# Kernel optimization log

Measured on AMD Instinct MI355X. Metric: run time of the kernel, lower is better.

## Reference

```python
import jax, jax.numpy as jnp
import numpy as np

TEMPERATURE = 0.5
NEG_INF = -1e9  # used to mask self-similarity diagonal before logsumexp


def setup_inputs() -> dict:
    key = jax.random.key(0)
    k1, k2 = jax.random.split(key)
    N, Z = 4096, 128
    z1 = jax.random.normal(k1, (N, Z), dtype=jnp.float32)
    z2 = jax.random.normal(k2, (N, Z), dtype=jnp.float32)
    return {"z1": z1, "z2": z2}


def reference(z1, z2):
    # NT-Xent (SimCLR) loss. Faithful to:
    #   sim = cosine_similarity over all pairs of concat([z1, z2])
    #   positives = sim diagonals at offsets +-N; negatives = all off-(self)diag entries
    #   cross_entropy with the positive as class 0  ->  -pos/T + logsumexp(all non-self sims / T)
    N = z1.shape[0]
    reps = jnp.concatenate([z1, z2], axis=0)                      # [2N, Z]
    # row-normalize once; cosine sim matrix is then a single GEMM
    norms = jnp.linalg.norm(reps, axis=-1, keepdims=True)
    # torch cosine_similarity clamps norms by eps=1e-8
    nreps = reps / jnp.maximum(norms, 1e-8)
    sim = nreps @ nreps.T                                          # [2N, 2N]
    # positives: sim[i, i+N] for i<N and sim[i, i-N] for i>=N
    l_pos = jnp.diagonal(sim, offset=N)                            # [N]
    r_pos = jnp.diagonal(sim, offset=-N)                           # [N]
    positives = jnp.concatenate([l_pos, r_pos])                    # [2N]
    # logsumexp over all entries except the self-similarity diagonal.
    # (The positive entry stays in the denominator exactly once, matching
    #  concat([positive, negatives]) in the original.)
    two_n = 2 * N
    self_mask = jnp.eye(two_n, dtype=bool)
    logits = jnp.where(self_mask, NEG_INF, sim / TEMPERATURE)      # [2N, 2N]
    lse = jax.nn.logsumexp(logits, axis=1)                         # [2N]
    per_row = lse - positives / TEMPERATURE                        # CE with label 0
    return jnp.sum(per_row) / two_n
```

## Files before the change

kernel.cpp:

```cpp
#include <hip/hip_runtime.h>
#include <hip/hip_bf16.h>


#define N_PAIRS 4096
#define ZDIM    128
#define NROWS   8192
#define EXP_SCALE 2.8853900817779268f

typedef __bf16 bf16x8 __attribute__((ext_vector_type(8)));
typedef float  floatx4 __attribute__((ext_vector_type(4)));

__global__ __launch_bounds__(256) void k_zero(float* __restrict__ denom) {
    int i = blockIdx.x * 256 + threadIdx.x;
    if (i < NROWS) denom[i] = 0.0f;
}

__global__ __launch_bounds__(256) void k_normalize(
    const float* __restrict__ z1, const float* __restrict__ z2,
    __hip_bfloat16* __restrict__ nreps, float* __restrict__ pos)
{
    const int w = threadIdx.x >> 6;
    const int lane = threadIdx.x & 63;
    const int p = blockIdx.x * 4 + w;
    const float2 a = ((const float2*)(z1 + (size_t)p * ZDIM))[lane];
    const float2 b = ((const float2*)(z2 + (size_t)p * ZDIM))[lane];
    float s1 = a.x * a.x + a.y * a.y;
    float s2 = b.x * b.x + b.y * b.y;
    float d  = a.x * b.x + a.y * b.y;
    #pragma unroll
    for (int off = 1; off < 64; off <<= 1) {
        s1 += __shfl_xor(s1, off, 64);
        s2 += __shfl_xor(s2, off, 64);
        d  += __shfl_xor(d,  off, 64);
    }
    const float n1 = fmaxf(sqrtf(s1), 1e-8f);
    const float n2 = fmaxf(sqrtf(s2), 1e-8f);
    const float i1 = 1.0f / n1, i2 = 1.0f / n2;
    float2 na; na.x = a.x * i1; na.y = a.y * i1;
    float2 nb; nb.x = b.x * i2; nb.y = b.y * i2;
    ((__hip_bfloat162*)(nreps + (size_t)p * ZDIM))[lane] = __float22bfloat162_rn(na);
    ((__hip_bfloat162*)(nreps + (size_t)(p + N_PAIRS) * ZDIM))[lane] = __float22bfloat162_rn(nb);
    if (lane == 0) pos[p] = d * i1 * i2;
}

__global__ __launch_bounds__(256, 2) void k_simsum(
    const __hip_bfloat16* __restrict__ nreps, float* __restrict__ denom)
{
    const int tid  = threadIdx.x;
    const int lane = tid & 63;
    const int w    = tid >> 6;
    const int wr   = w >> 1, wc = w & 1;
    const int rt   = blockIdx.x >> 3;
    const int cs   = blockIdx.x & 7;
    const int q    = lane >> 4;
    const int l16  = lane & 15;

    const int arow = rt * 128 + wr * 64 + l16;
    const __hip_bfloat16* Abase = nreps + (size_t)arow * ZDIM + q * 8;
    bf16x8 afrag[4][4];
    #pragma unroll
    for (int mt = 0; mt < 4; ++mt)
        #pragma unroll
        for (int ks = 0; ks < 4; ++ks)
            afrag[mt][ks] = *(const bf16x8*)(Abase + mt * 16 * ZDIM + ks * 32);

    float rowsum[4][4];
    #pragma unroll
    for (int mt = 0; mt < 4; ++mt)
        #pragma unroll
        for (int r = 0; r < 4; ++r) rowsum[mt][r] = 0.0f;

    const int colbase = cs * 1024 + wc * 64 + l16;
    const int growb   = rt * 128 + wr * 64 + q * 4;

    for (int it = 0; it < 8; ++it) {
        floatx4 acc[4][4];
        #pragma unroll
        for (int mt = 0; mt < 4; ++mt)
            #pragma unroll
            for (int nt = 0; nt < 4; ++nt) {
                acc[mt][nt].x = 0.f; acc[mt][nt].y = 0.f;
                acc[mt][nt].z = 0.f; acc[mt][nt].w = 0.f;
            }
        const __hip_bfloat16* Bbase =
            nreps + (size_t)(colbase + it * 128) * ZDIM + q * 8;
        #pragma unroll
        for (int ks = 0; ks < 4; ++ks) {
            bf16x8 bfrag[4];
            #pragma unroll
            for (int nt = 0; nt < 4; ++nt)
                bfrag[nt] = *(const bf16x8*)(Bbase + nt * 16 * ZDIM + ks * 32);
            #pragma unroll
            for (int mt = 0; mt < 4; ++mt)
                #pragma unroll
                for (int nt = 0; nt < 4; ++nt)
                    acc[mt][nt] = __builtin_amdgcn_mfma_f32_16x16x32_bf16(
                        afrag[mt][ks], bfrag[nt], acc[mt][nt], 0, 0, 0);
        }
        const int gcolb = cs * 1024 + it * 128 + wc * 64 + l16;
        #pragma unroll
        for (int mt = 0; mt < 4; ++mt) {
            #pragma unroll
            for (int nt = 0; nt < 4; ++nt) {
                const int gcol = gcolb + nt * 16;
                #pragma unroll
                for (int r = 0; r < 4; ++r) {
                    const int grow = growb + mt * 16 + r;
                    const float e = __expf(acc[mt][nt][r] * 2.0f);
                    rowsum[mt][r] += (grow == gcol) ? 0.0f : e;
                }
            }
        }
    }

    #pragma unroll
    for (int mt = 0; mt < 4; ++mt)
        #pragma unroll
        for (int r = 0; r < 4; ++r) {
            float s = rowsum[mt][r];
            s += __shfl_xor(s, 1, 64);
            s += __shfl_xor(s, 2, 64);
            s += __shfl_xor(s, 4, 64);
            s += __shfl_xor(s, 8, 64);
            rowsum[mt][r] = s;
        }
    if (l16 == 0) {
        #pragma unroll
        for (int mt = 0; mt < 4; ++mt)
            #pragma unroll
            for (int r = 0; r < 4; ++r) {
                const int grow = rt * 128 + wr * 64 + mt * 16 + q * 4 + r;
                atomicAdd(&denom[grow], rowsum[mt][r]);
            }
    }
}

__global__ __launch_bounds__(1024) void k_finish(
    const float* __restrict__ denom, const float* __restrict__ pos,
    float* __restrict__ out)
{
    __shared__ float red[1024];
    const int t = threadIdx.x;
    float s = 0.0f;
    for (int i = t; i < NROWS; i += 1024) s += __logf(denom[i]);
    float p = 0.0f;
    for (int i = t; i < N_PAIRS; i += 1024) p += pos[i];
    red[t] = s - 4.0f * p;
    __syncthreads();
    for (int off = 512; off > 0; off >>= 1) {
        if (t < off) red[t] += red[t + off];
        __syncthreads();
    }
    if (t == 0) out[0] = red[0] / (float)NROWS;
}

extern "C" void kernel_launch(void* const* d_in, const int* in_sizes, int n_in,
                              void* d_out, int out_size, void* d_ws, size_t ws_size,
                              hipStream_t stream) {
    const float* z1 = (const float*)d_in[0];
    const float* z2 = (const float*)d_in[1];
    float* out = (float*)d_out;

    char* ws = (char*)d_ws;
    __hip_bfloat16* nreps = (__hip_bfloat16*)ws;
    float* denom = (float*)(ws + (size_t)NROWS * ZDIM * 2);
    float* pos   = denom + NROWS;

    k_zero<<<NROWS / 256, 256, 0, stream>>>(denom);
    k_normalize<<<N_PAIRS / 4, 256, 0, stream>>>(z1, z2, nreps, pos);
    k_simsum<<<512, 256, 0, stream>>>(nreps, denom);
    k_finish<<<1, 1024, 0, stream>>>(denom, pos, out);
}
```

Measured before the change: 102.2 us.

## Fold exp2 scale into normalization, fuse zeroing, halve simsum tiles for occupancy

Pre-scales normalized rows by sqrt(2/ln2) so the GEMM output feeds exp2 directly, removing the per-element multiply. The diagonal mask is now applied only on tiles that contain the diagonal. The separate zero kernel is merged into normalize, which drops one launch. The simsum grid doubles with half-width column tiles and launch bounds allow 3 blocks per CU, aiming for more occupancy. The trade-off is some extra bf16 rounding from the scaled values and more atomics.

```diff
diff --git a/kernel.cpp b/kernel.cpp
--- a/kernel.cpp
+++ b/kernel.cpp
@@ -5,20 +5,19 @@
 #define N_PAIRS 4096
 #define ZDIM    128
 #define NROWS   8192
-#define EXP_SCALE 2.8853900817779268f
+#define QS 1.6986437717f
 
 typedef __bf16 bf16x8 __attribute__((ext_vector_type(8)));
 typedef float  floatx4 __attribute__((ext_vector_type(4)));
 
-__global__ __launch_bounds__(256) void k_zero(float* __restrict__ denom) {
-    int i = blockIdx.x * 256 + threadIdx.x;
-    if (i < NROWS) denom[i] = 0.0f;
-}
-
 __global__ __launch_bounds__(256) void k_normalize(
     const float* __restrict__ z1, const float* __restrict__ z2,
-    __hip_bfloat16* __restrict__ nreps, float* __restrict__ pos)
+    __hip_bfloat16* __restrict__ nreps, float* __restrict__ pos,
+    float* __restrict__ denom)
 {
+    const int zi = blockIdx.x * 256 + threadIdx.x;
+    if (zi < NROWS) denom[zi] = 0.0f;
+
     const int w = threadIdx.x >> 6;
     const int lane = threadIdx.x & 63;
     const int p = blockIdx.x * 4 + w;
@@ -36,27 +35,28 @@
     const float n1 = fmaxf(sqrtf(s1), 1e-8f);
     const float n2 = fmaxf(sqrtf(s2), 1e-8f);
     const float i1 = 1.0f / n1, i2 = 1.0f / n2;
-    float2 na; na.x = a.x * i1; na.y = a.y * i1;
-    float2 nb; nb.x = b.x * i2; nb.y = b.y * i2;
+    const float q1 = i1 * QS, q2 = i2 * QS;
+    float2 na; na.x = a.x * q1; na.y = a.y * q1;
+    float2 nb; nb.x = b.x * q2; nb.y = b.y * q2;
     ((__hip_bfloat162*)(nreps + (size_t)p * ZDIM))[lane] = __float22bfloat162_rn(na);
     ((__hip_bfloat162*)(nreps + (size_t)(p + N_PAIRS) * ZDIM))[lane] = __float22bfloat162_rn(nb);
     if (lane == 0) pos[p] = d * i1 * i2;
 }
 
-__global__ __launch_bounds__(256, 2) void k_simsum(
+__global__ __launch_bounds__(256, 3) void k_simsum(
     const __hip_bfloat16* __restrict__ nreps, float* __restrict__ denom)
 {
     const int tid  = threadIdx.x;
     const int lane = tid & 63;
     const int w    = tid >> 6;
     const int wr   = w >> 1, wc = w & 1;
-    const int rt   = blockIdx.x >> 3;
-    const int cs   = blockIdx.x & 7;
+    const int rt   = blockIdx.x >> 4;
+    const int cs   = blockIdx.x & 15;
     const int q    = lane >> 4;
     const int l16  = lane & 15;
 
-    const int arow = rt * 128 + wr * 64 + l16;
-    const __hip_bfloat16* Abase = nreps + (size_t)arow * ZDIM + q * 8;
+    const int arowb = rt * 128 + wr * 64;
+    const __hip_bfloat16* Abase = nreps + (size_t)(arowb + l16) * ZDIM + q * 8;
     bf16x8 afrag[4][4];
     #pragma unroll
     for (int mt = 0; mt < 4; ++mt)
@@ -70,44 +70,46 @@
         #pragma unroll
         for (int r = 0; r < 4; ++r) rowsum[mt][r] = 0.0f;
 
-    const int colbase = cs * 1024 + wc * 64 + l16;
-    const int growb   = rt * 128 + wr * 64 + q * 4;
-
     for (int it = 0; it < 8; ++it) {
-        floatx4 acc[4][4];
+        floatx4 acc[4][2];
         #pragma unroll
         for (int mt = 0; mt < 4; ++mt)
             #pragma unroll
-            for (int nt = 0; nt < 4; ++nt) {
+            for (int nt = 0; nt < 2; ++nt) {
                 acc[mt][nt].x = 0.f; acc[mt][nt].y = 0.f;
                 acc[mt][nt].z = 0.f; acc[mt][nt].w = 0.f;
             }
-        const __hip_bfloat16* Bbase =
-            nreps + (size_t)(colbase + it * 128) * ZDIM + q * 8;
+        const int colb = cs * 512 + it * 64 + wc * 32;
+        const __hip_bfloat16* Bbase = nreps + (size_t)(colb + l16) * ZDIM + q * 8;
         #pragma unroll
         for (int ks = 0; ks < 4; ++ks) {
-            bf16x8 bfrag[4];
+            bf16x8 bfrag[2];
             #pragma unroll
-            for (int nt = 0; nt < 4; ++nt)
+            for (int nt = 0; nt < 2; ++nt)
                 bfrag[nt] = *(const bf16x8*)(Bbase + nt * 16 * ZDIM + ks * 32);
             #pragma unroll
             for (int mt = 0; mt < 4; ++mt)
                 #pragma unroll
-                for (int nt = 0; nt < 4; ++nt)
+                for (int nt = 0; nt < 2; ++nt)
                     acc[mt][nt] = __builtin_amdgcn_mfma_f32_16x16x32_bf16(
                         afrag[mt][ks], bfrag[nt], acc[mt][nt], 0, 0, 0);
         }
-        const int gcolb = cs * 1024 + it * 128 + wc * 64 + l16;
         #pragma unroll
         for (int mt = 0; mt < 4; ++mt) {
+            const int rowtb = arowb + mt * 16;
             #pragma unroll
-            for (int nt = 0; nt < 4; ++nt) {
-                const int gcol = gcolb + nt * 16;
-                #pragma unroll
-                for (int r = 0; r < 4; ++r) {
-                    const int grow = growb + mt * 16 + r;
-                    const float e = __expf(acc[mt][nt][r] * 2.0f);
-                    rowsum[mt][r] += (grow == gcol) ? 0.0f : e;
+            for (int nt = 0; nt < 2; ++nt) {
+                const int coltb = colb + nt * 16;
+                if (rowtb == coltb) {
+                    #pragma unroll
+                    for (int r = 0; r < 4; ++r) {
+                        const float e = __builtin_amdgcn_exp2f(acc[mt][nt][r]);
+                        rowsum[mt][r] += (l16 == q * 4 + r) ? 0.0f : e;
+                    }
+                } else {
+                    #pragma unroll
+                    for (int r = 0; r < 4; ++r)
+                        rowsum[mt][r] += __builtin_amdgcn_exp2f(acc[mt][nt][r]);
                 }
             }
         }
@@ -129,7 +131,7 @@
         for (int mt = 0; mt < 4; ++mt)
             #pragma unroll
             for (int r = 0; r < 4; ++r) {
-                const int grow = rt * 128 + wr * 64 + mt * 16 + q * 4 + r;
+                const int grow = arowb + mt * 16 + q * 4 + r;
                 atomicAdd(&denom[grow], rowsum[mt][r]);
             }
     }
@@ -166,8 +168,7 @@
     float* denom = (float*)(ws + (size_t)NROWS * ZDIM * 2);
     float* pos   = denom + NROWS;
 
-    k_zero<<<NROWS / 256, 256, 0, stream>>>(denom);
-    k_normalize<<<N_PAIRS / 4, 256, 0, stream>>>(z1, z2, nreps, pos);
-    k_simsum<<<512, 256, 0, stream>>>(nreps, denom);
+    k_normalize<<<N_PAIRS / 4, 256, 0, stream>>>(z1, z2, nreps, pos, denom);
+    k_simsum<<<1024, 256, 0, stream>>>(nreps, denom);
     k_finish<<<1, 1024, 0, stream>>>(denom, pos, out);
 }
```

Result: slower. 155.9 us (+52.6%).
